# Kernel optimization log

Hardware: AMD Instinct MI355X
Metric: run time of the kernel (lower is better)

The kernel has to match this reference:

```python
import jax, jax.numpy as jnp
import numpy as np

B, N, D_PATCH = 32, 196, 768
TKN, QK, H, HID = 768, 64, 12, 3072
K_STEPS = 12
ALPHA = 1.0
BETA = 1.0 / (QK ** 0.5)
EPS = 1e-5


def setup_inputs() -> dict:
    key = jax.random.key(0)
    ks = jax.random.split(key, 8)
    w_std = 0.002
    return {
        "x": jax.random.normal(ks[0], (B, N, D_PATCH), jnp.float32),
        "w_enc": jax.random.normal(ks[1], (TKN, D_PATCH), jnp.float32) * 0.02,
        "b_enc": jnp.zeros((TKN,), jnp.float32),
        "cls_tok": jnp.ones((1, 1, TKN), jnp.float32),
        "pos": jax.random.normal(ks[2], (1, N + 1, TKN), jnp.float32) * w_std,
        "eln_gamma": jnp.ones((1,), jnp.float32),
        "eln_bias": jnp.zeros((TKN,), jnp.float32),
        "wq": jax.random.normal(ks[3], (H, QK, TKN), jnp.float32) * w_std,
        "wk": jax.random.normal(ks[4], (H, QK, TKN), jnp.float32) * w_std,
        "w_hop": jax.random.normal(ks[5], (HID, TKN), jnp.float32) * 0.02,
        "dec_ln_w": jnp.ones((TKN,), jnp.float32),
        "dec_ln_b": jnp.zeros((TKN,), jnp.float32),
        "w_dec": jax.random.normal(ks[6], (D_PATCH, TKN), jnp.float32) * 0.02,
        "b_dec": jnp.zeros((D_PATCH,), jnp.float32),
    }


def _energy(g, wq, wk, w_hop):
    # attention energy: non-softmax, -1/beta * sum logsumexp(beta * A)
    q = jnp.einsum('bnd,hzd->bnhz', g, wq)
    k = jnp.einsum('bnd,hzd->bnhz', g, wk)
    A = jnp.einsum('bqhz,bkhz->bhqk', q, k)  # [B,H,N+1,N+1]
    e_attn = (-1.0 / BETA) * jnp.sum(jax.nn.logsumexp(BETA * A, axis=-1))
    # Hopfield energy: -0.5 * sum relu(g W^T)^2
    h = jnp.einsum('bnd,fd->bnf', g, w_hop)  # [B,N+1,HID]
    e_hop = -0.5 * jnp.sum(jax.nn.relu(h) ** 2)
    return e_attn + e_hop


def _energy_ln(x, gamma, bias):
    xm = x - x.mean(-1, keepdims=True)
    o = xm / jnp.sqrt((xm ** 2).mean(-1, keepdims=True) + EPS)
    return gamma * o + bias


def _layernorm(x, w, b):
    mu = x.mean(-1, keepdims=True)
    xm = x - mu
    var = (xm ** 2).mean(-1, keepdims=True)
    return xm / jnp.sqrt(var + EPS) * w + b


def reference(x, w_enc, b_enc, cls_tok, pos, eln_gamma, eln_bias,
              wq, wk, w_hop, dec_ln_w, dec_ln_b, w_dec, b_dec):
    # encode: Linear(d_patch -> tkn)
    t = jnp.einsum('bnd,td->bnt', x, w_enc) + b_enc
    # prepend cls, add positional encoding
    cls = jnp.broadcast_to(cls_tok, (t.shape[0], 1, TKN))
    t = jnp.concatenate([cls, t], axis=1) + pos  # [B, N+1, TKN]

    grad_e = jax.grad(lambda g: _energy(g, wq, wk, w_hop))
    for _ in range(K_STEPS):  # fixed unroll over time steps (single block)
        g = _energy_ln(t, eln_gamma, eln_bias)
        t = t - ALPHA * grad_e(g)

    # decode: LayerNorm + Linear(tkn -> d_patch)
    y = _layernorm(t, dec_ln_w, dec_ln_b)
    y = jnp.einsum('bnt,dt->bnd', y, w_dec) + b_dec
    return y[:, 1:]  # drop cls token (use_cls=False)
```

## Files before the change

### kernel.cpp

```cpp
#include <hip/hip_runtime.h>
#include <hip/hip_bf16.h>

typedef __hip_bfloat16 bf16;
typedef short s8 __attribute__((ext_vector_type(8)));
typedef short sv4 __attribute__((ext_vector_type(4)));
typedef float f4 __attribute__((ext_vector_type(4)));

#define BETA 0.125f
#define EPS 1e-5f

__device__ __forceinline__ void gld16(const void* g, void* l){
    __builtin_amdgcn_global_load_lds(
        (const __attribute__((address_space(1))) void*)g,
        (__attribute__((address_space(3))) void*)l, 16, 0, 0);
}

__global__ __launch_bounds__(256) void pre_k(
    const float* __restrict__ wq, const float* __restrict__ wk, const float* __restrict__ w_hop,
    const float* __restrict__ w_enc, const float* __restrict__ w_dec,
    const float* __restrict__ x, const float* __restrict__ cls, const float* __restrict__ pos,
    bf16* __restrict__ B1, bf16* __restrict__ we_, bf16* __restrict__ wd_,
    bf16* __restrict__ g_, float* __restrict__ t_)
{
    long e = (long)blockIdx.x*256 + threadIdx.x;
    if (e < 3538944L){
        float v;
        if (e < 589824L)        v = wq[e];
        else if (e < 1179648L)  v = wk[e - 589824L];
        else                    v = w_hop[e - 1179648L];
        B1[e] = __float2bfloat16(v);
    } else if (e < 4128768L){
        long i = e - 3538944L;  we_[i] = __float2bfloat16(w_enc[i]);
    } else if (e < 4718592L){
        long i = e - 4128768L;  wd_[i] = __float2bfloat16(w_dec[i]);
    } else if (e < 9633792L){
        long i = e - 4718592L;
        long row = i / 768;
        g_[i] = (row < 6272) ? __float2bfloat16(x[i]) : __float2bfloat16(0.f);
    } else {
        long i = e - 9633792L;
        int b = (int)(i / 768), c = (int)(i % 768);
        if (b < 32) t_[((long)b*197)*768 + c] = cls[c] + pos[c];
    }
}

__global__ __launch_bounds__(256) void tr_k(const short* __restrict__ Bi, short* __restrict__ Bo){
    __shared__ short t[32][33];
    int i0 = blockIdx.x*32, j0 = blockIdx.y*32;
    int li = threadIdx.x & 31, lj = threadIdx.x >> 5;
    #pragma unroll
    for (int r=0;r<4;r++) t[lj+8*r][li] = Bi[(long)(i0+lj+8*r)*768 + j0+li];
    __syncthreads();
    #pragma unroll
    for (int r=0;r<4;r++) Bo[(long)(j0+lj+8*r)*4608 + i0+li] = t[li][lj+8*r];
}

template<int MODE>
__global__ __launch_bounds__(256) void big_gemm(
    const short* __restrict__ A, int lda,
    const short* __restrict__ B, int ldb,
    float* __restrict__ Cf, bf16* __restrict__ Cb, int ldc,
    int K, int Nn, int Nm, int relu0, long zoff,
    const float* __restrict__ bias, const float* __restrict__ pos)
{
    const int f = blockIdx.x;
    const int npg = 16*Nn;
    const int grp = f / npg;
    const int first_m = grp*16;
    const int gs = (Nm - first_m < 16) ? (Nm - first_m) : 16;
    const int rem = f % npg;
    const int bm = first_m + rem % gs;
    const int bn = rem / gs;

    __shared__ short lsA[8192];
    __shared__ short lsB[8192];
    const int tid = threadIdx.x;
    const int w = tid>>6, l = tid&63;
    const int m0 = bm*128, n0 = bn*128;
    const int srow = tid>>2;
    const int qglob = ((tid&3) - (tid>>3)) & 3;
    const int scol = qglob*8;
    int koff, Ks;
    if (MODE==1){ Ks = K>>1; koff = blockIdx.z * Ks; Cf += (size_t)blockIdx.z * zoff; }
    else        { Ks = K;    koff = 0; }
    const short* pa = A + (size_t)(m0+srow)*lda + koff + scol;
    const short* pb = B + (size_t)(n0+srow)*ldb + koff + scol;
    short* laP = lsA + w*512;
    short* lbP = lsB + w*512;
    const int wm = (w>>1)*64, wn = (w&1)*64;
    const int fr = l&15, fq = ((l>>4) + (fr>>1) & 3)*8;
    f4 acc[4][4] = {};
    const int nk = Ks>>6;
    for (int kt=0; kt<nk; kt++){
        const size_t ko = (size_t)kt*64;
        const size_t ra = 64*(size_t)lda, rb = 64*(size_t)ldb;
        gld16(pa + ko,           laP);
        gld16(pa + ko + ra,      laP + 2048);
        gld16(pa + ko + 32,      laP + 4096);
        gld16(pa + ko + 32 + ra, laP + 6144);
        gld16(pb + ko,           lbP);
        gld16(pb + ko + rb,      lbP + 2048);
        gld16(pb + ko + 32,      lbP + 4096);
        gld16(pb + ko + 32 + rb, lbP + 6144);
        __syncthreads();
        #pragma unroll
        for (int ks=0; ks<2; ks++){
            s8 af[4], bfr[4];
            #pragma unroll
            for (int i=0;i<4;i++) af[i]  = *(const s8*)(lsA + ks*4096 + (wm+i*16+fr)*32 + fq);
            #pragma unroll
            for (int j=0;j<4;j++) bfr[j] = *(const s8*)(lsB + ks*4096 + (wn+j*16+fr)*32 + fq);
            #pragma unroll
            for (int i=0;i<4;i++)
                #pragma unroll
                for (int j=0;j<4;j++)
                    acc[i][j] = __builtin_amdgcn_mfma_f32_16x16x32_bf16(af[i], bfr[j], acc[i][j], 0,0,0);
        }
        __syncthreads();
    }
    const int er = (l>>4)*4;
    const int ec = l&15;
    #pragma unroll
    for (int i=0;i<4;i++){
        #pragma unroll
        for (int j=0;j<4;j++){
            int gr0 = m0 + wm + i*16 + er;
            int gc  = n0 + wn + j*16 + ec;
            #pragma unroll
            for (int r=0;r<4;r++){
                float v = acc[i][j][r];
                int gr = gr0 + r;
                if (MODE==0){
                    if (gc >= relu0) v = v>0.f ? v : 0.f;
                    Cb[(size_t)gr*ldc + gc] = __float2bfloat16(v);
                } else if (MODE==1){
                    Cf[(size_t)gr*ldc + gc] = v;
                } else if (MODE==2){
                    if (gr < 6272){
                        int b = gr/196, n = gr%196;
                        Cf[((size_t)b*197 + n + 1)*768 + gc] = v + bias[gc] + pos[(long)(n+1)*768+gc];
                    }
                } else {
                    if (gr < 6272) Cf[(size_t)gr*ldc + gc] = v + bias[gc];
                }
            }
        }
    }
}

template<int MODE>
__global__ __launch_bounds__(256, 2) void wide_gemm(
    const short* __restrict__ A, int lda,
    const short* __restrict__ B, int ldb,
    float* __restrict__ Cf, float* __restrict__ Cf2,
    bf16* __restrict__ Cb, int ldc,
    int K, int Nn, int Nm, int relu0, long zoff)
{
    const int f = blockIdx.x;
    const int npg = 16*Nn;
    const int grp = f / npg;
    const int first_m = grp*16;
    const int gs = (Nm - first_m < 16) ? (Nm - first_m) : 16;
    const int rem = f % npg;
    const int bm = first_m + rem % gs;
    const int bn = rem / gs;

    __shared__ short lsA[16384];
    __shared__ short lsB[8192];
    const int tid = threadIdx.x;
    const int w = tid>>6, l = tid&63;
    const int m0 = bm*256, n0 = bn*128;

    int Ks, koff; float* Cp = Cf;
    if (MODE==1){ Ks = K/3; koff = blockIdx.z * Ks;
                  Cp = (blockIdx.z==2) ? Cf2 : Cf + (size_t)blockIdx.z * zoff; }
    else        { Ks = K; koff = 0; }
    const int NT = Ks>>6;

    const short* sA[4]; const short* sB[2];
    #pragma unroll
    for (int j=0;j<4;j++){
        int c = j*256 + tid;
        int r = (c>>2)&255, qd = c&3;
        int qs = (qd - (r>>1)) & 3;
        sA[j] = A + (size_t)(m0+r)*lda + koff + qs*8;
    }
    #pragma unroll
    for (int j=0;j<2;j++){
        int c = j*256 + tid;
        int r = (c>>2)&127, qd = c&3;
        int qs = (qd - (r>>1)) & 3;
        sB[j] = B + (size_t)(n0+r)*ldb + koff + qs*8;
    }

    const int wm = (w>>1)*128, wn = (w&1)*64;
    const int fr = l&15;
    const int fq = (((l>>4) + (fr>>1)) & 3)*8;
    f4 acc[8][4] = {};

    for (int kt=0; kt<NT; kt++){
        const size_t ko = (size_t)kt*64;
        short* dA = lsA + w*512;
        short* dB = lsB + w*512;
        #pragma unroll
        for (int j=0;j<4;j++){
            gld16(sA[j]+ko,      dA + j*2048);
            gld16(sA[j]+ko+32,   dA + (j+4)*2048);
        }
        #pragma unroll
        for (int j=0;j<2;j++){
            gld16(sB[j]+ko,      dB + j*2048);
            gld16(sB[j]+ko+32,   dB + (j+2)*2048);
        }
        __syncthreads();
        #pragma unroll
        for (int ks=0; ks<2; ks++){
            s8 af[8], bfr[4];
            #pragma unroll
            for (int i=0;i<8;i++) af[i]  = *(const s8*)(lsA + ks*8192 + (wm+i*16+fr)*32 + fq);
            #pragma unroll
            for (int j=0;j<4;j++) bfr[j] = *(const s8*)(lsB + ks*4096 + (wn+j*16+fr)*32 + fq);
            #pragma unroll
            for (int i=0;i<8;i++)
                #pragma unroll
                for (int j=0;j<4;j++)
                    acc[i][j] = __builtin_amdgcn_mfma_f32_16x16x32_bf16(af[i], bfr[j], acc[i][j], 0,0,0);
        }
        __syncthreads();
    }

    const int er = (l>>4)*4;
    const int ec = l&15;
    #pragma unroll
    for (int i=0;i<8;i++){
        #pragma unroll
        for (int j=0;j<4;j++){
            int gr0 = m0 + wm + i*16 + er;
            int gc  = n0 + wn + j*16 + ec;
            #pragma unroll
            for (int r=0;r<4;r++){
                float v = acc[i][j][r];
                int gr = gr0 + r;
                if (MODE==0){
                    if (gc >= relu0) v = v>0.f ? v : 0.f;
                    Cb[(size_t)gr*ldc + gc] = __float2bfloat16(v);
                } else {
                    Cp[(size_t)gr*ldc + gc] = v;
                }
            }
        }
    }
}

__global__ __launch_bounds__(256) void pack_k(const short* __restrict__ qkh,
                                              short* __restrict__ qT, short* __restrict__ kT){
    __shared__ short tq[64][65];
    __shared__ short tk[64][65];
    const int bh = blockIdx.x, b = bh/12, h = bh%12;
    const int mc = blockIdx.y*64;
    const int tid = threadIdx.x;
    #pragma unroll
    for (int e=0;e<16;e++){
        int i = tid + e*256; int r = i>>6, c = i&63;
        int mg = mc + r;
        short vq = 0, vk = 0;
        if (mg < 197){
            size_t base = (size_t)(b*197+mg)*4608 + h*64 + c;
            vq = qkh[base]; vk = qkh[base+768];
        }
        tq[r][c] = vq; tk[r][c] = vk;
    }
    __syncthreads();
    #pragma unroll
    for (int e=0;e<16;e++){
        int i = tid + e*256; int zr = i>>6, cm = i&63;
        size_t o = (size_t)bh*16384 + (size_t)zr*256 + mc + cm;
        qT[o] = tq[cm][zr];
        kT[o] = tk[cm][zr];
    }
}

__global__ __launch_bounds__(256) void attn_k(
    short* __restrict__ qkh, const short* __restrict__ qT, const short* __restrict__ kT)
{
    __shared__ short Pl[64*232];
    __shared__ short Ptl[208*72];
    const int bh = blockIdx.x, b = bh/12, h = bh%12;
    const int tid = threadIdx.x, w = tid>>6, l = tid&63;
    const int lr = l&15, lq = l>>4;
    const size_t qcol = (size_t)h*64, kcol = 768 + qcol;
    const size_t rbase = (size_t)b*197*4608;
    const short* qTp = qT + (size_t)bh*16384;
    const short* kTp = kT + (size_t)bh*16384;

    for (int i=tid; i<64*16; i+=256){ int r=i>>4, c=208+(i&15); Pl[r*232+c]=0; }

    f4 ak[13];
    #pragma unroll
    for (int t=0;t<13;t++) ak[t] = (f4){0.f,0.f,0.f,0.f};

    for (int iter=0; iter<4; iter++){
        const int m0 = iter*64;
        f4 S[13];
        #pragma unroll
        for (int t=0;t<13;t++) S[t] = (f4){0.f,0.f,0.f,0.f};
        const int mrow = m0 + w*16 + lr;
        #pragma unroll
        for (int ks=0; ks<2; ks++){
            s8 af = *(const s8*)(qkh + rbase + (size_t)mrow*4608 + qcol + ks*32 + lq*8);
            #pragma unroll
            for (int t=0;t<13;t++){
                s8 bf = *(const s8*)(qkh + rbase + (size_t)(t*16+lr)*4608 + kcol + ks*32 + lq*8);
                S[t] = __builtin_amdgcn_mfma_f32_16x16x32_bf16(af, bf, S[t], 0,0,0);
            }
        }
        __syncthreads();
        const int mbase = w*16 + lq*4;
        #pragma unroll
        for (int r=0;r<4;r++){
            float mx = -1e30f;
            #pragma unroll
            for (int t=0;t<13;t++){
                float v = S[t][r]*BETA;
                if (t==12 && lr>=5) v = -1e30f;
                S[t][r] = v;
                mx = fmaxf(mx, v);
            }
            mx = fmaxf(mx, __shfl_xor(mx,1,64)); mx = fmaxf(mx, __shfl_xor(mx,2,64));
            mx = fmaxf(mx, __shfl_xor(mx,4,64)); mx = fmaxf(mx, __shfl_xor(mx,8,64));
            float sm = 0.f;
            #pragma unroll
            for (int t=0;t<13;t++){ float e = __expf(S[t][r]-mx); S[t][r]=e; sm+=e; }
            sm += __shfl_xor(sm,1,64); sm += __shfl_xor(sm,2,64);
            sm += __shfl_xor(sm,4,64); sm += __shfl_xor(sm,8,64);
            float inv = 1.f/sm;
            bool valid = (m0 + mbase + r) < 197;
            #pragma unroll
            for (int t=0;t<13;t++) S[t][r] = valid ? S[t][r]*inv : 0.f;
        }
        #pragma unroll
        for (int t=0;t<13;t++){
            int c = t*16 + lr;
            short pb[4];
            #pragma unroll
            for (int r=0;r<4;r++){
                bf16 bv = __float2bfloat16(S[t][r]);
                pb[r] = *(short*)&bv;
                Pl[(mbase+r)*232 + c] = pb[r];
            }
            *(sv4*)(Ptl + c*72 + mbase) = (sv4){pb[0],pb[1],pb[2],pb[3]};
        }
        __syncthreads();
        f4 aq[4];
        #pragma unroll
        for (int t=0;t<4;t++) aq[t] = (f4){0.f,0.f,0.f,0.f};
        #pragma unroll
        for (int ks=0; ks<7; ks++){
            s8 af = *(const s8*)(kTp + (w*16+lr)*256 + ks*32 + lq*8);
            #pragma unroll
            for (int mt=0;mt<4;mt++){
                s8 bf = *(const s8*)(Pl + (mt*16+lr)*232 + ks*32 + lq*8);
                aq[mt] = __builtin_amdgcn_mfma_f32_16x16x32_bf16(af, bf, aq[mt], 0,0,0);
            }
        }
        #pragma unroll
        for (int mt=0;mt<4;mt++){
            int mg = m0 + mt*16 + lr;
            if (mg < 197){
                sv4 pv;
                #pragma unroll
                for (int r=0;r<4;r++){ bf16 bv=__float2bfloat16(aq[mt][r]); pv[r]=*(short*)&bv; }
                *(sv4*)(qkh + rbase + (size_t)mg*4608 + qcol + w*16 + lq*4) = pv;
            }
        }
        #pragma unroll
        for (int ks=0; ks<2; ks++){
            s8 bf = *(const s8*)(qTp + (w*16+lr)*256 + m0 + ks*32 + lq*8);
            #pragma unroll
            for (int t=0;t<13;t++){
                s8 af = *(const s8*)(Ptl + (t*16+lr)*72 + ks*32 + lq*8);
                ak[t] = __builtin_amdgcn_mfma_f32_16x16x32_bf16(af, bf, ak[t], 0,0,0);
            }
        }
    }
    #pragma unroll
    for (int t=0;t<13;t++){
        #pragma unroll
        for (int r=0;r<4;r++){
            int n = t*16 + lq*4 + r;
            if (n < 197)
                *(bf16*)(qkh + rbase + (size_t)n*4608 + kcol + w*16 + lr) = __float2bfloat16(ak[t][r]);
        }
    }
}

__global__ __launch_bounds__(192) void ln_k(
    float* __restrict__ in, bf16* __restrict__ out,
    const float* __restrict__ p0, const float* __restrict__ p1, const float* __restrict__ p2,
    const float* __restrict__ scale, const float* __restrict__ bias,
    int scalar_scale, int rowmap, int addp, int writet)
{
    int r = blockIdx.x;
    long src = rowmap ? ((long)(r/196)*197 + r%196 + 1) : (long)r;
    float4* xr = (float4*)(in + src*768);
    int tid = threadIdx.x;
    float4 v = xr[tid];
    if (addp){
        float4 a = ((const float4*)(p0 + src*768))[tid];
        float4 b = ((const float4*)(p1 + src*768))[tid];
        float4 c = ((const float4*)(p2 + src*768))[tid];
        v.x += a.x + b.x + c.x;
        v.y += a.y + b.y + c.y;
        v.z += a.z + b.z + c.z;
        v.w += a.w + b.w + c.w;
        if (writet) xr[tid] = v;
    }
    __shared__ float red[3];
    float s = v.x + v.y + v.z + v.w;
    #pragma unroll
    for (int o=1;o<64;o<<=1) s += __shfl_xor(s, o, 64);
    if ((tid&63)==0) red[tid>>6] = s;
    __syncthreads();
    float mu = (red[0]+red[1]+red[2]) * (1.f/768.f);
    float dx = v.x-mu, dy = v.y-mu, dz = v.z-mu, dw = v.w-mu;
    float q = dx*dx + dy*dy + dz*dz + dw*dw;
    #pragma unroll
    for (int o=1;o<64;o<<=1) q += __shfl_xor(q, o, 64);
    __syncthreads();
    if ((tid&63)==0) red[tid>>6] = q;
    __syncthreads();
    float ms = (red[0]+red[1]+red[2]) * (1.f/768.f);
    float inv = rsqrtf(ms + EPS);
    float4 s4, b4;
    if (scalar_scale){ float s0 = scale[0]; s4 = make_float4(s0,s0,s0,s0); }
    else              s4 = ((const float4*)scale)[tid];
    b4 = ((const float4*)bias)[tid];
    bf16 o0 = __float2bfloat16(dx*inv*s4.x + b4.x);
    bf16 o1 = __float2bfloat16(dy*inv*s4.y + b4.y);
    bf16 o2 = __float2bfloat16(dz*inv*s4.z + b4.z);
    bf16 o3 = __float2bfloat16(dw*inv*s4.w + b4.w);
    *(sv4*)(out + (long)r*768 + tid*4) =
        (sv4){*(short*)&o0, *(short*)&o1, *(short*)&o2, *(short*)&o3};
}

extern "C" void kernel_launch(void* const* d_in, const int* in_sizes, int n_in,
                              void* d_out, int out_size, void* d_ws, size_t ws_size,
                              hipStream_t stream) {
    const float* x       = (const float*)d_in[0];
    const float* w_enc   = (const float*)d_in[1];
    const float* b_enc   = (const float*)d_in[2];
    const float* cls_tok = (const float*)d_in[3];
    const float* pos     = (const float*)d_in[4];
    const float* eln_g   = (const float*)d_in[5];
    const float* eln_b   = (const float*)d_in[6];
    const float* wq      = (const float*)d_in[7];
    const float* wk      = (const float*)d_in[8];
    const float* w_hop   = (const float*)d_in[9];
    const float* dln_w   = (const float*)d_in[10];
    const float* dln_b   = (const float*)d_in[11];
    const float* w_dec   = (const float*)d_in[12];
    const float* b_dec   = (const float*)d_in[13];
    float* out = (float*)d_out;

    float* t_  = (float*)d_ws;
    bf16* g_   = (bf16*)(t_ + 6400L*768);
    bf16* qkh  = g_ + 6400L*768;
    bf16* qT   = qkh + 6400L*4608;
    bf16* kT   = qT + 384L*16384;
    float* p0  = (float*)(kT + 384L*16384);
    float* p1  = p0 + 6400L*768;
    bf16* B1   = (bf16*)(p1 + 6400L*768);
    bf16* B2   = B1 + 4608L*768;
    bf16* we_  = B2 + 768L*4608;
    bf16* wd_  = we_ + 768L*768;
    float* p2  = (float*)qT;

    dim3 blk(256);
    dim3 lblk(192);
    const long ZOFF = 6400L*768;

    pre_k<<<dim3(37728), blk, 0, stream>>>(wq, wk, w_hop, w_enc, w_dec, x, cls_tok, pos,
                                           B1, we_, wd_, g_, t_);
    tr_k<<<dim3(144,24), blk, 0, stream>>>((const short*)B1, (short*)B2);

    big_gemm<2><<<dim3(300), blk, 0, stream>>>((const short*)g_, 768, (const short*)we_, 768,
                                               t_, nullptr, 768, 768, 6, 50, 0, 0, b_enc, pos);

    for (int step=0; step<12; step++){
        ln_k<<<dim3(6304), lblk, 0, stream>>>(t_, g_, p0, p1, p2, eln_g, eln_b, 1, 0, step>0, 1);
        wide_gemm<0><<<dim3(900), blk, 0, stream>>>((const short*)g_, 768, (const short*)B1, 768,
                                                    nullptr, nullptr, qkh, 4608, 768, 36, 25, 1536, 0);
        pack_k<<<dim3(384,4), blk, 0, stream>>>((const short*)qkh, (short*)qT, (short*)kT);
        attn_k<<<dim3(384), blk, 0, stream>>>((short*)qkh, (const short*)qT, (const short*)kT);
        wide_gemm<1><<<dim3(150,1,3), blk, 0, stream>>>((const short*)qkh, 4608, (const short*)B2, 4608,
                                                        p0, p2, nullptr, 768, 4608, 6, 25, 0, ZOFF);
    }

    ln_k<<<dim3(6272), lblk, 0, stream>>>(t_, g_, p0, p1, p2, dln_w, dln_b, 0, 1, 1, 0);
    big_gemm<3><<<dim3(300), blk, 0, stream>>>((const short*)g_, 768, (const short*)wd_, 768,
                                               out, nullptr, 768, 768, 6, 50, 0, 0, b_dec, nullptr);
}
```

Measured before the change: 2.383 ms.

## Split attention query tiles across two warp groups with LDS reduction

The attention kernel now runs 512 threads per (batch, head) block instead of 256. Two groups of four waves each process alternate 64-row query tiles, using double-sized LDS buffers. Their partial key-gradient accumulators are summed through shared memory before the write. This doubles per-block parallelism across only 384 blocks, at the cost of more LDS use, an extra reduction step and barriers.

Result: no change. 2.423 ms (+1.7%).

```diff
diff --git a/kernel.cpp b/kernel.cpp
--- a/kernel.cpp
+++ b/kernel.cpp
@@ -280,31 +280,38 @@
     }
 }
 
-__global__ __launch_bounds__(256) void attn_k(
+__global__ __launch_bounds__(512) void attn_k(
     short* __restrict__ qkh, const short* __restrict__ qT, const short* __restrict__ kT)
 {
-    __shared__ short Pl[64*232];
-    __shared__ short Ptl[208*72];
+    __shared__ short Pl[2*64*232];
+    __shared__ short Ptl[2*208*72];
     const int bh = blockIdx.x, b = bh/12, h = bh%12;
     const int tid = threadIdx.x, w = tid>>6, l = tid&63;
+    const int wl = w & 3, grp = w >> 2;
     const int lr = l&15, lq = l>>4;
     const size_t qcol = (size_t)h*64, kcol = 768 + qcol;
     const size_t rbase = (size_t)b*197*4608;
     const short* qTp = qT + (size_t)bh*16384;
     const short* kTp = kT + (size_t)bh*16384;
-
-    for (int i=tid; i<64*16; i+=256){ int r=i>>4, c=208+(i&15); Pl[r*232+c]=0; }
+    short* Plg  = Pl  + grp*(64*232);
+    short* Ptlg = Ptl + grp*(208*72);
+
+    for (int i=tid; i<2*64*16; i+=512){
+        int buf = i >> 10, rem = i & 1023;
+        int r = rem>>4, c = 208 + (rem&15);
+        Pl[buf*(64*232) + r*232 + c] = 0;
+    }
 
     f4 ak[13];
     #pragma unroll
     for (int t=0;t<13;t++) ak[t] = (f4){0.f,0.f,0.f,0.f};
 
-    for (int iter=0; iter<4; iter++){
-        const int m0 = iter*64;
+    for (int it=0; it<2; it++){
+        const int m0 = (it*2 + grp)*64;
         f4 S[13];
         #pragma unroll
         for (int t=0;t<13;t++) S[t] = (f4){0.f,0.f,0.f,0.f};
-        const int mrow = m0 + w*16 + lr;
+        const int mrow = m0 + wl*16 + lr;
         #pragma unroll
         for (int ks=0; ks<2; ks++){
             s8 af = *(const s8*)(qkh + rbase + (size_t)mrow*4608 + qcol + ks*32 + lq*8);
@@ -315,7 +322,7 @@
             }
         }
         __syncthreads();
-        const int mbase = w*16 + lq*4;
+        const int mbase = wl*16 + lq*4;
         #pragma unroll
         for (int r=0;r<4;r++){
             float mx = -1e30f;
@@ -346,9 +353,9 @@
             for (int r=0;r<4;r++){
                 bf16 bv = __float2bfloat16(S[t][r]);
                 pb[r] = *(short*)&bv;
-                Pl[(mbase+r)*232 + c] = pb[r];
-            }
-            *(sv4*)(Ptl + c*72 + mbase) = (sv4){pb[0],pb[1],pb[2],pb[3]};
+                Plg[(mbase+r)*232 + c] = pb[r];
+            }
+            *(sv4*)(Ptlg + c*72 + mbase) = (sv4){pb[0],pb[1],pb[2],pb[3]};
         }
         __syncthreads();
         f4 aq[4];
@@ -356,10 +363,10 @@
         for (int t=0;t<4;t++) aq[t] = (f4){0.f,0.f,0.f,0.f};
         #pragma unroll
         for (int ks=0; ks<7; ks++){
-            s8 af = *(const s8*)(kTp + (w*16+lr)*256 + ks*32 + lq*8);
+            s8 af = *(const s8*)(kTp + (wl*16+lr)*256 + ks*32 + lq*8);
             #pragma unroll
             for (int mt=0;mt<4;mt++){
-                s8 bf = *(const s8*)(Pl + (mt*16+lr)*232 + ks*32 + lq*8);
+                s8 bf = *(const s8*)(Plg + (mt*16+lr)*232 + ks*32 + lq*8);
                 aq[mt] = __builtin_amdgcn_mfma_f32_16x16x32_bf16(af, bf, aq[mt], 0,0,0);
             }
         }
@@ -370,26 +377,40 @@
                 sv4 pv;
                 #pragma unroll
                 for (int r=0;r<4;r++){ bf16 bv=__float2bfloat16(aq[mt][r]); pv[r]=*(short*)&bv; }
-                *(sv4*)(qkh + rbase + (size_t)mg*4608 + qcol + w*16 + lq*4) = pv;
+                *(sv4*)(qkh + rbase + (size_t)mg*4608 + qcol + wl*16 + lq*4) = pv;
             }
         }
         #pragma unroll
         for (int ks=0; ks<2; ks++){
-            s8 bf = *(const s8*)(qTp + (w*16+lr)*256 + m0 + ks*32 + lq*8);
+            s8 bf = *(const s8*)(qTp + (wl*16+lr)*256 + m0 + ks*32 + lq*8);
             #pragma unroll
             for (int t=0;t<13;t++){
-                s8 af = *(const s8*)(Ptl + (t*16+lr)*72 + ks*32 + lq*8);
+                s8 af = *(const s8*)(Ptlg + (t*16+lr)*72 + ks*32 + lq*8);
                 ak[t] = __builtin_amdgcn_mfma_f32_16x16x32_bf16(af, bf, ak[t], 0,0,0);
             }
         }
     }
-    #pragma unroll
-    for (int t=0;t<13;t++){
-        #pragma unroll
-        for (int r=0;r<4;r++){
-            int n = t*16 + lq*4 + r;
-            if (n < 197)
-                *(bf16*)(qkh + rbase + (size_t)n*4608 + kcol + w*16 + lr) = __float2bfloat16(ak[t][r]);
+
+    __syncthreads();
+    float* F = (float*)Ptl;
+    if (grp == 1){
+        #pragma unroll
+        for (int t=0;t<13;t++)
+            #pragma unroll
+            for (int r=0;r<4;r++)
+                F[(t*16+lq*4+r)*68 + wl*16 + lr] = ak[t][r];
+    }
+    __syncthreads();
+    if (grp == 0){
+        #pragma unroll
+        for (int t=0;t<13;t++){
+            #pragma unroll
+            for (int r=0;r<4;r++){
+                float v = ak[t][r] + F[(t*16+lq*4+r)*68 + wl*16 + lr];
+                int n = t*16 + lq*4 + r;
+                if (n < 197)
+                    *(bf16*)(qkh + rbase + (size_t)n*4608 + kcol + wl*16 + lr) = __float2bfloat16(v);
+            }
         }
     }
 }
@@ -491,7 +512,7 @@
         wide_gemm<0><<<dim3(900), blk, 0, stream>>>((const short*)g_, 768, (const short*)B1, 768,
                                                     nullptr, nullptr, qkh, 4608, 768, 36, 25, 1536, 0);
         pack_k<<<dim3(384,4), blk, 0, stream>>>((const short*)qkh, (short*)qT, (short*)kT);
-        attn_k<<<dim3(384), blk, 0, stream>>>((short*)qkh, (const short*)qT, (const short*)kT);
+        attn_k<<<dim3(384), dim3(512), 0, stream>>>((short*)qkh, (const short*)qT, (const short*)kT);
         wide_gemm<1><<<dim3(150,1,3), blk, 0, stream>>>((const short*)qkh, 4608, (const short*)B2, 4608,
                                                         p0, p2, nullptr, 768, 4608, 6, 25, 0, ZOFF);
     }
```
